# Kernel optimization log

Hardware: AMD Instinct MI355X
Metric: run time of the kernel (lower is better)

## Reference

```python
import jax, jax.numpy as jnp
import numpy as np

N_NODES = 100000
N_EDGES = 800000
N_GRAPHS = 4000
EMB = 128      # node_emb_dims
HID = 256      # hidden_dims
FP = 2048      # fingerprint_dims
FIELD_DIMS = {"atom_type": 120, "degree": 12, "charge": 10}


def setup_inputs() -> dict:
    key = jax.random.key(0)
    ks = iter(jax.random.split(key, 40))
    p = lambda shape: jax.random.normal(next(ks), shape, dtype=jnp.float32) * 0.02
    inp = {
        "atom_idx": jax.random.randint(next(ks), (N_NODES,), 0, FIELD_DIMS["atom_type"]),
        "degree_idx": jax.random.randint(next(ks), (N_NODES,), 0, FIELD_DIMS["degree"]),
        "charge_idx": jax.random.randint(next(ks), (N_NODES,), 0, FIELD_DIMS["charge"]),
        "edge_index": jax.random.randint(next(ks), (2, N_EDGES), 0, N_NODES),
        "batch": jnp.sort(jax.random.randint(next(ks), (N_NODES,), 0, N_GRAPHS)),
        "fingerprint": jax.random.normal(next(ks), (N_GRAPHS, FP), dtype=jnp.float32),
        # FFM projector params
        "emb_atom": p((FIELD_DIMS["atom_type"], EMB)),
        "emb_degree": p((FIELD_DIMS["degree"], EMB)),
        "emb_charge": p((FIELD_DIMS["charge"], EMB)),
        "proj_w1": p((3 * EMB, EMB)), "proj_b1": jnp.zeros((EMB,), jnp.float32),
        "proj_w2": p((EMB, EMB)), "proj_b2": jnp.zeros((EMB,), jnp.float32),
        # fingerprint linear
        "fp_w": p((FP, HID)), "fp_b": jnp.zeros((HID,), jnp.float32),
        # GCN layers
        "conv_w0": p((EMB, HID)), "conv_b0": jnp.zeros((HID,), jnp.float32),
        "conv_w1": p((HID, HID)), "conv_b1": jnp.zeros((HID,), jnp.float32),
        "conv_w2": p((HID, HID)), "conv_b2": jnp.zeros((HID,), jnp.float32),
        "conv_w3": p((HID, HID)), "conv_b3": jnp.zeros((HID,), jnp.float32),
        # head
        "lin1_w": p((2 * HID, HID // 2)), "lin1_b": jnp.zeros((HID // 2,), jnp.float32),
        "lin2_w": p((HID // 2, 1)), "lin2_b": jnp.zeros((1,), jnp.float32),
    }
    return inp


def gcn_conv(x, w, b, src, dst, n):
    # PyG GCNConv: linear, add self-loops, symmetric norm, scatter-add at dst, + bias
    xw = x @ w
    loop = jnp.arange(n)
    src_f = jnp.concatenate([src, loop])
    dst_f = jnp.concatenate([dst, loop])
    deg = jax.ops.segment_sum(jnp.ones_like(dst_f, dtype=x.dtype), dst_f, num_segments=n)
    dinv = jax.lax.rsqrt(deg)  # deg >= 1 thanks to self-loops
    norm = dinv[src_f] * dinv[dst_f]                       # [E+N]
    msg = xw[src_f] * norm[:, None]                        # [E+N, HID]
    return jax.ops.segment_sum(msg, dst_f, num_segments=n) + b


def reference(atom_idx, degree_idx, charge_idx, edge_index, batch, fingerprint,
              emb_atom, emb_degree, emb_charge,
              proj_w1, proj_b1, proj_w2, proj_b2, fp_w, fp_b,
              conv_w0, conv_b0, conv_w1, conv_b1, conv_w2, conv_b2, conv_w3, conv_b3,
              lin1_w, lin1_b, lin2_w, lin2_b):
    # FieldAwareFactorizationMachine projector (vectorized over all nodes)
    e = jnp.concatenate([emb_atom[atom_idx], emb_degree[degree_idx], emb_charge[charge_idx]], axis=-1)
    h = jax.nn.relu(e @ proj_w1 + proj_b1) @ proj_w2 + proj_b2   # [N, EMB]
    src, dst = edge_index[0], edge_index[1]
    for w, b in ((conv_w0, conv_b0), (conv_w1, conv_b1), (conv_w2, conv_b2), (conv_w3, conv_b3)):
        h = jax.nn.relu(gcn_conv(h, w, b, src, dst, N_NODES))
    pooled = jax.ops.segment_sum(h, batch, num_segments=N_GRAPHS)  # scatter sum pooling
    fp_emb = fingerprint @ fp_w + fp_b
    z = jnp.concatenate([fp_emb, pooled], axis=-1)                 # [B, 2*HID]
    z = jax.nn.relu(z @ lin1_w + lin1_b)
    return z @ lin2_w + lin2_b                                     # [B, 1]
```

## Files before the change

### kernel.cpp

```cpp
#include <hip/hip_runtime.h>
#include <stdint.h>

#define NN 100000
#define NE 800000
#define NG 4000
#define NBLK ((NN + 255) / 256)

typedef __attribute__((ext_vector_type(8))) short s16x8;
typedef __attribute__((ext_vector_type(4))) float f32x4;

__device__ __forceinline__ float b2f(unsigned short u) {
    return __uint_as_float(((unsigned int)u) << 16);
}
__device__ __forceinline__ unsigned short f2b(float f) {
    unsigned int x = __float_as_uint(f);
    x = x + 0x7FFFu + ((x >> 16) & 1u);
    return (unsigned short)(x >> 16);
}
__device__ __forceinline__ s16x8 cvt8(const float* __restrict__ p) {
    float4 a = *(const float4*)p;
    float4 b = *(const float4*)(p + 4);
    s16x8 r = {(short)f2b(a.x), (short)f2b(a.y), (short)f2b(a.z), (short)f2b(a.w),
               (short)f2b(b.x), (short)f2b(b.y), (short)f2b(b.z), (short)f2b(b.w)};
    return r;
}

__device__ __forceinline__ void gload16(const void* g, void* l) {
    __builtin_amdgcn_global_load_lds((const __attribute__((address_space(1))) unsigned int*)g,
                                     (__attribute__((address_space(3))) unsigned int*)l, 16, 0, 0);
}

__global__ void k_count(const int* __restrict__ dst, int* __restrict__ cnt) {
    int e = blockIdx.x * 256 + threadIdx.x;
    if (e < NE) atomicAdd(&cnt[dst[e]], 1);
}

__global__ void k_dinv(const int* __restrict__ cnt, float* __restrict__ dinv) {
    int n = blockIdx.x * 256 + threadIdx.x;
    if (n < NN) dinv[n] = rsqrtf((float)(cnt[n] + 1));
}

__global__ __launch_bounds__(256) void k_bsum(const int* __restrict__ cnt, int* __restrict__ bsum) {
    __shared__ int s[256];
    int i = blockIdx.x * 256 + threadIdx.x;
    s[threadIdx.x] = (i < NN) ? cnt[i] : 0;
    __syncthreads();
    for (int off = 128; off; off >>= 1) {
        if (threadIdx.x < off) s[threadIdx.x] += s[threadIdx.x + off];
        __syncthreads();
    }
    if (threadIdx.x == 0) bsum[blockIdx.x] = s[0];
}

__global__ __launch_bounds__(512) void k_bscan(const int* __restrict__ bsum, int* __restrict__ bpre) {
    __shared__ int s[512];
    int t = threadIdx.x;
    int v = (t < NBLK) ? bsum[t] : 0;
    s[t] = v;
    __syncthreads();
    for (int off = 1; off < 512; off <<= 1) {
        int u = (t >= off) ? s[t - off] : 0;
        __syncthreads();
        s[t] += u;
        __syncthreads();
    }
    if (t < NBLK) bpre[t] = s[t] - v;
}

__global__ __launch_bounds__(256) void k_rowptr(const int* __restrict__ cnt, const int* __restrict__ bpre,
                                                int* __restrict__ row_ptr, int* __restrict__ cursor) {
    __shared__ int s[256];
    int t = threadIdx.x;
    int i = blockIdx.x * 256 + t;
    int v = (i < NN) ? cnt[i] : 0;
    s[t] = v;
    __syncthreads();
    for (int off = 1; off < 256; off <<= 1) {
        int u = (t >= off) ? s[t - off] : 0;
        __syncthreads();
        s[t] += u;
        __syncthreads();
    }
    if (i < NN) {
        int excl = bpre[blockIdx.x] + s[t] - v;
        row_ptr[i] = excl;
        cursor[i] = excl;
        if (i == NN - 1) row_ptr[NN] = NE;
    }
}

__global__ void k_fill(const int* __restrict__ src, const int* __restrict__ dst,
                       int* __restrict__ cursor, int* __restrict__ colA) {
    int e = blockIdx.x * 256 + threadIdx.x;
    if (e < NE) {
        int d = dst[e];
        int p = atomicAdd(&cursor[d], 1);
        colA[p] = src[e];
    }
}

__global__ void k_t(const float* __restrict__ src, unsigned short* __restrict__ dst, int KN, int ln) {
    int i = blockIdx.x * 256 + threadIdx.x;
    if (i < KN) {
        int k = i >> ln, n = i & ((1 << ln) - 1);
        dst[(size_t)n * (KN >> ln) + k] = f2b(src[i]);
    }
}

__global__ void k_cvt(const float* __restrict__ src, unsigned short* __restrict__ dst, int n8) {
    int i = blockIdx.x * 256 + threadIdx.x;
    if (i < n8) *(s16x8*)&dst[(size_t)i * 8] = cvt8(&src[(size_t)i * 8]);
}

__global__ void k_binit(float* __restrict__ fe, const float* __restrict__ b) {
    int i = blockIdx.x * 256 + threadIdx.x;
    fe[i] = b[i & 255];
}

__global__ void k_z(const float* __restrict__ fe, unsigned short* __restrict__ zcat) {
    int i = blockIdx.x * 256 + threadIdx.x;
    int g = i >> 8, c = i & 255;
    zcat[(size_t)g * 512 + c] = f2b(fe[i]);
}

template <bool GATHER, bool BIAS, bool RELU, bool CBF16>
__global__ __launch_bounds__(256) void k_mm(
    const unsigned short* __restrict__ A, const unsigned short* __restrict__ Bt,
    void* __restrict__ Cv, const float* __restrict__ bias, int M, int N, int K,
    const int* __restrict__ ai, const int* __restrict__ di, const int* __restrict__ ci,
    const float* __restrict__ ea, const float* __restrict__ ed, const float* __restrict__ ec) {
    __shared__ unsigned short As[128 * 40];
    __shared__ unsigned short Bs[128 * 40];
    const int tid = threadIdx.x;
    const int row0 = blockIdx.x * 128, col0 = blockIdx.y * 128;
    const int lane = tid & 63, wid = tid >> 6;
    const int wrow = (wid >> 1) * 64, wcol = (wid & 1) * 64;
    const int lr = lane & 15, lk8 = (lane >> 4) * 8;

    const int sr = tid >> 1;
    const int skc = (tid & 1) * 16;
    const int agrow = row0 + sr;
    const int bgrow = col0 + sr;
    int ia = 0, idg = 0, ic = 0;
    if (GATHER && agrow < M) { ia = ai[agrow] * 128; idg = di[agrow] * 128; ic = ci[agrow] * 128; }

    f32x4 acc[4][4] = {};

    for (int kb = 0; kb < K; kb += 32) {
        if (kb) __syncthreads();
#pragma unroll
        for (int c = 0; c < 2; ++c) {
            int kloc = skc + c * 8;
            s16x8 v = {};
            if (agrow < M) {
                if (GATHER) {
                    int kg = kb + kloc;
                    const float* p = (kg < 128) ? (ea + ia + kg)
                                   : (kg < 256) ? (ed + idg + kg - 128)
                                                : (ec + ic + kg - 256);
                    v = cvt8(p);
                } else {
                    v = *(const s16x8*)&A[(size_t)agrow * K + kb + kloc];
                }
            }
            *(s16x8*)&As[sr * 40 + kloc] = v;
            s16x8 w = *(const s16x8*)&Bt[(size_t)bgrow * K + kb + kloc];
            *(s16x8*)&Bs[sr * 40 + kloc] = w;
        }
        __syncthreads();
        s16x8 af[4], bfr[4];
#pragma unroll
        for (int f = 0; f < 4; ++f)
            af[f] = *(const s16x8*)&As[(wrow + f * 16 + lr) * 40 + lk8];
#pragma unroll
        for (int f = 0; f < 4; ++f)
            bfr[f] = *(const s16x8*)&Bs[(wcol + f * 16 + lr) * 40 + lk8];
#pragma unroll
        for (int fm = 0; fm < 4; ++fm)
#pragma unroll
            for (int fn = 0; fn < 4; ++fn)
                acc[fm][fn] = __builtin_amdgcn_mfma_f32_16x16x32_bf16(af[fm], bfr[fn], acc[fm][fn], 0, 0, 0);
    }
#pragma unroll
    for (int fm = 0; fm < 4; ++fm) {
#pragma unroll
        for (int r = 0; r < 4; ++r) {
            int row = row0 + wrow + fm * 16 + (lane >> 4) * 4 + r;
            if (row < M) {
#pragma unroll
                for (int fn = 0; fn < 4; ++fn) {
                    int col = col0 + wcol + fn * 16 + lr;
                    float v = acc[fm][fn][r];
                    if (BIAS) v += bias[col];
                    if (RELU) v = fmaxf(v, 0.f);
                    if (CBF16) ((unsigned short*)Cv)[(size_t)row * N + col] = f2b(v);
                    else       ((float*)Cv)[(size_t)row * N + col] = v;
                }
            }
        }
    }
}

template <bool BIAS, bool RELU, bool CBF16, bool SPLITK>
__global__ __launch_bounds__(256) void k_mmA(
    const unsigned short* __restrict__ A, const unsigned short* __restrict__ Bt,
    void* __restrict__ Cv, const float* __restrict__ bias, int M, int N, int K, int kc) {
    __shared__ unsigned short As[128 * 32];
    __shared__ unsigned short Bs[128 * 32];
    const int tid = threadIdx.x;
    const int row0 = blockIdx.x * 128, col0 = blockIdx.y * 128;
    const int lane = tid & 63, wid = tid >> 6;
    const int wrow = (wid >> 1) * 64, wcol = (wid & 1) * 64;
    const int lr = lane & 15, lk8 = (lane >> 4) * 8;

    const int k0 = SPLITK ? blockIdx.z * kc : 0;
    const int k1 = SPLITK ? k0 + kc : K;

    const int sra = wid * 32 + (lane >> 2);
    const int sca = (lane & 3) * 8;
    const unsigned short* a0 = A + (size_t)min(row0 + sra, M - 1) * K + sca;
    const unsigned short* a1 = A + (size_t)min(row0 + sra + 16, M - 1) * K + sca;
    const unsigned short* b0 = Bt + (size_t)(col0 + sra) * K + sca;
    const unsigned short* b1 = Bt + (size_t)(col0 + sra + 16) * K + sca;
    unsigned short* lA0 = &As[(wid * 2 + 0) * 512];
    unsigned short* lA1 = &As[(wid * 2 + 1) * 512];
    unsigned short* lB0 = &Bs[(wid * 2 + 0) * 512];
    unsigned short* lB1 = &Bs[(wid * 2 + 1) * 512];

    f32x4 acc[4][4] = {};

    for (int kb = k0; kb < k1; kb += 32) {
        if (kb != k0) __syncthreads();
        gload16(a0 + kb, lA0);
        gload16(a1 + kb, lA1);
        gload16(b0 + kb, lB0);
        gload16(b1 + kb, lB1);
        __syncthreads();
        s16x8 af[4], bfr[4];
#pragma unroll
        for (int f = 0; f < 4; ++f)
            af[f] = *(const s16x8*)&As[(wrow + f * 16 + lr) * 32 + lk8];
#pragma unroll
        for (int f = 0; f < 4; ++f)
            bfr[f] = *(const s16x8*)&Bs[(wcol + f * 16 + lr) * 32 + lk8];
#pragma unroll
        for (int fm = 0; fm < 4; ++fm)
#pragma unroll
            for (int fn = 0; fn < 4; ++fn)
                acc[fm][fn] = __builtin_amdgcn_mfma_f32_16x16x32_bf16(af[fm], bfr[fn], acc[fm][fn], 0, 0, 0);
    }
#pragma unroll
    for (int fm = 0; fm < 4; ++fm) {
#pragma unroll
        for (int r = 0; r < 4; ++r) {
            int row = row0 + wrow + fm * 16 + (lane >> 4) * 4 + r;
            if (row < M) {
#pragma unroll
                for (int fn = 0; fn < 4; ++fn) {
                    int col = col0 + wcol + fn * 16 + lr;
                    float v = acc[fm][fn][r];
                    if (SPLITK) {
                        atomicAdd(&((float*)Cv)[(size_t)row * N + col], v);
                    } else {
                        if (BIAS) v += bias[col];
                        if (RELU) v = fmaxf(v, 0.f);
                        if (CBF16) ((unsigned short*)Cv)[(size_t)row * N + col] = f2b(v);
                        else       ((float*)Cv)[(size_t)row * N + col] = v;
                    }
                }
            }
        }
    }
}

template <int W, bool FUSE>
__global__ __launch_bounds__(256) void k_scat(const unsigned short* __restrict__ xw,
                                              unsigned short* __restrict__ hout,
                                              const float* __restrict__ dinv,
                                              const int* __restrict__ row_ptr,
                                              const int* __restrict__ colA,
                                              const float* __restrict__ bias) {
    constexpr int RPW = 1024 / W;
    constexpr int G = 64 / RPW;
    const int wid = threadIdx.x >> 6, lane = threadIdx.x & 63;
    const int v = blockIdx.x * 4 + wid;
    const int grp = lane / G, li = lane % G;
    const int c0 = li * 8;
    const float dv = dinv[v];
    float acc[8] = {};
    const int beg = row_ptr[v], end = row_ptr[v + 1];
    int p = beg + grp;
    for (; p + RPW < end; p += 2 * RPW) {
        int s0 = colA[p], s1 = colA[p + RPW];
        float w0 = dinv[s0] * dv, w1 = dinv[s1] * dv;
        s16x8 r0 = *(const s16x8*)&xw[(size_t)s0 * W + c0];
        s16x8 r1 = *(const s16x8*)&xw[(size_t)s1 * W + c0];
#pragma unroll
        for (int j = 0; j < 8; ++j) acc[j] = fmaf(b2f((unsigned short)r0[j]), w0, acc[j]);
#pragma unroll
        for (int j = 0; j < 8; ++j) acc[j] = fmaf(b2f((unsigned short)r1[j]), w1, acc[j]);
    }
    if (p < end) {
        int s0 = colA[p];
        float w0 = dinv[s0] * dv;
        s16x8 r0 = *(const s16x8*)&xw[(size_t)s0 * W + c0];
#pragma unroll
        for (int j = 0; j < 8; ++j) acc[j] = fmaf(b2f((unsigned short)r0[j]), w0, acc[j]);
    }
#pragma unroll
    for (int j = 0; j < 8; ++j) {
        if (RPW == 4) acc[j] += __shfl_xor(acc[j], 16);
        acc[j] += __shfl_xor(acc[j], 32);
    }
    s16x8 rs = *(const s16x8*)&xw[(size_t)v * W + c0];
    const float ws = dv * dv;
    unsigned short o[8];
#pragma unroll
    for (int j = 0; j < 8; ++j) {
        float x = fmaf(b2f((unsigned short)rs[j]), ws, acc[j]);
        if (FUSE) x = fmaxf(x + bias[c0 + j], 0.f);
        o[j] = f2b(x);
    }
    if (grp == 0) *(s16x8*)&hout[(size_t)v * W + c0] = *(const s16x8*)o;
}

__global__ __launch_bounds__(256) void k_scat256(const unsigned short* __restrict__ xw,
                                                 unsigned short* __restrict__ hout,
                                                 const float* __restrict__ dinv,
                                                 const int* __restrict__ row_ptr,
                                                 const int* __restrict__ colA,
                                                 const float* __restrict__ bias) {
    const int wid = threadIdx.x >> 6, lane = threadIdx.x & 63;
    const int v = blockIdx.x * 2 + (wid >> 1);
    const int cs = (wid & 1) * 128;
    const int grp = lane >> 4, li = lane & 15;
    const int c0 = cs + li * 8;
    const float dv = dinv[v];
    float acc[8] = {};
    const int beg = row_ptr[v], end = row_ptr[v + 1];
    int p = beg + grp;
    for (; p + 4 < end; p += 8) {
        int s0 = colA[p], s1 = colA[p + 4];
        float w0 = dinv[s0] * dv, w1 = dinv[s1] * dv;
        s16x8 r0 = *(const s16x8*)&xw[(size_t)s0 * 256 + c0];
        s16x8 r1 = *(const s16x8*)&xw[(size_t)s1 * 256 + c0];
#pragma unroll
        for (int j = 0; j < 8; ++j) acc[j] = fmaf(b2f((unsigned short)r0[j]), w0, acc[j]);
#pragma unroll
        for (int j = 0; j < 8; ++j) acc[j] = fmaf(b2f((unsigned short)r1[j]), w1, acc[j]);
    }
    if (p < end) {
        int s0 = colA[p];
        float w0 = dinv[s0] * dv;
        s16x8 r0 = *(const s16x8*)&xw[(size_t)s0 * 256 + c0];
#pragma unroll
        for (int j = 0; j < 8; ++j) acc[j] = fmaf(b2f((unsigned short)r0[j]), w0, acc[j]);
    }
#pragma unroll
    for (int j = 0; j < 8; ++j) {
        acc[j] += __shfl_xor(acc[j], 16);
        acc[j] += __shfl_xor(acc[j], 32);
    }
    s16x8 rs = *(const s16x8*)&xw[(size_t)v * 256 + c0];
    const float ws = dv * dv;
    unsigned short o[8];
#pragma unroll
    for (int j = 0; j < 8; ++j) {
        float x = fmaf(b2f((unsigned short)rs[j]), ws, acc[j]);
        x = fmaxf(x + bias[c0 + j], 0.f);
        o[j] = f2b(x);
    }
    if (grp == 0) *(s16x8*)&hout[(size_t)v * 256 + c0] = *(const s16x8*)o;
}

__global__ void k_bounds(const int* __restrict__ batch, int* __restrict__ gstart) {
    int n = blockIdx.x * 256 + threadIdx.x;
    if (n >= NN) return;
    int b = batch[n];
    if (n == 0) {
        for (int g = 0; g <= b; ++g) gstart[g] = 0;
    } else {
        int pb = batch[n - 1];
        if (pb != b)
            for (int g = pb + 1; g <= b; ++g) gstart[g] = n;
    }
    if (n == NN - 1) {
        for (int g = b + 1; g <= NG; ++g) gstart[g] = NN;
    }
}

__global__ __launch_bounds__(64) void k_pool(const unsigned short* __restrict__ h,
                                             const int* __restrict__ gstart,
                                             unsigned short* __restrict__ zcat) {
    int g = blockIdx.x;
    int lane = threadIdx.x;
    int c0 = lane * 4;
    int beg = gstart[g], end = gstart[g + 1];
    float a0 = 0.f, a1 = 0.f, a2 = 0.f, a3 = 0.f;
    for (int n = beg; n < end; ++n) {
        ushort4 r = *(const ushort4*)&h[(size_t)n * 256 + c0];
        a0 += b2f(r.x); a1 += b2f(r.y); a2 += b2f(r.z); a3 += b2f(r.w);
    }
    ushort4 o;
    o.x = f2b(a0); o.y = f2b(a1); o.z = f2b(a2); o.w = f2b(a3);
    *(ushort4*)&zcat[(size_t)g * 512 + 256 + c0] = o;
}

__global__ __launch_bounds__(256) void k_dot(const float* __restrict__ z1,
                                             const float* __restrict__ w2,
                                             const float* __restrict__ b2,
                                             float* __restrict__ out) {
    int wid = threadIdx.x >> 6, lane = threadIdx.x & 63;
    int g = blockIdx.x * 4 + wid;
    float s = z1[(size_t)g * 128 + lane] * w2[lane]
            + z1[(size_t)g * 128 + 64 + lane] * w2[64 + lane];
#pragma unroll
    for (int off = 32; off; off >>= 1) s += __shfl_xor(s, off);
    if (lane == 0) out[g] = s + b2[0];
}

extern "C" void kernel_launch(void* const* d_in, const int* in_sizes, int n_in,
                              void* d_out, int out_size, void* d_ws, size_t ws_size,
                              hipStream_t stream) {
    const int* atom_idx   = (const int*)d_in[0];
    const int* degree_idx = (const int*)d_in[1];
    const int* charge_idx = (const int*)d_in[2];
    const int* edge_index = (const int*)d_in[3];
    const int* batch      = (const int*)d_in[4];
    const float* fingerprint = (const float*)d_in[5];
    const float* emb_atom   = (const float*)d_in[6];
    const float* emb_degree = (const float*)d_in[7];
    const float* emb_charge = (const float*)d_in[8];
    const float* proj_w1 = (const float*)d_in[9];
    const float* proj_b1 = (const float*)d_in[10];
    const float* proj_w2 = (const float*)d_in[11];
    const float* proj_b2 = (const float*)d_in[12];
    const float* fp_w = (const float*)d_in[13];
    const float* fp_b = (const float*)d_in[14];
    const float* conv_w[4] = {(const float*)d_in[15], (const float*)d_in[17],
                              (const float*)d_in[19], (const float*)d_in[21]};
    const float* conv_b[4] = {(const float*)d_in[16], (const float*)d_in[18],
                              (const float*)d_in[20], (const float*)d_in[22]};
    const float* lin1_w = (const float*)d_in[23];
    const float* lin1_b = (const float*)d_in[24];
    const float* lin2_w = (const float*)d_in[25];
    const float* lin2_b = (const float*)d_in[26];
    float* out = (float*)d_out;

    const int* src = edge_index;
    const int* dst = edge_index + NE;

    char* p = (char*)d_ws;
    auto carve = [&](size_t bytes) { void* r = (void*)p; p += (bytes + 255) & ~(size_t)255; return r; };
    unsigned short* bufA = (unsigned short*)carve((size_t)NN * 256 * 2);
    unsigned short* bufB = (unsigned short*)carve((size_t)NN * 256 * 2);
    int*   cnt     = (int*)carve((size_t)NN * 4);
    float* dinv    = (float*)carve((size_t)NN * 4);
    int*   row_ptr = (int*)carve((size_t)(NN + 1) * 4);
    int*   cursor  = (int*)carve((size_t)(NN + 1) * 4);
    int*   colA    = (int*)carve((size_t)NE * 4);
    int*   gstart  = (int*)carve((size_t)(NG + 1) * 4);
    float* fp_emb  = (float*)carve((size_t)NG * 256 * 4);
    int*   bsum    = (int*)carve((size_t)NBLK * 4);
    int*   bpre    = (int*)carve((size_t)NBLK * 4);
    unsigned short* w1t  = (unsigned short*)carve((size_t)128 * 384 * 2);
    unsigned short* w2t  = (unsigned short*)carve((size_t)128 * 128 * 2);
    unsigned short* cwt[4];
    cwt[0] = (unsigned short*)carve((size_t)256 * 128 * 2);
    for (int l = 1; l < 4; ++l) cwt[l] = (unsigned short*)carve((size_t)256 * 256 * 2);
    unsigned short* fpwt = (unsigned short*)carve((size_t)256 * 2048 * 2);
    unsigned short* fpbf = (unsigned short*)carve((size_t)NG * 2048 * 2);
    unsigned short* l1wt = (unsigned short*)carve((size_t)128 * 512 * 2);
    unsigned short* zcat = (unsigned short*)carve((size_t)NG * 512 * 2);
    float* z1      = (float*)carve((size_t)NG * 128 * 4);

    hipMemsetAsync(cnt, 0, (size_t)NN * 4, stream);
    k_count<<<(NE + 255) / 256, 256, 0, stream>>>(dst, cnt);
    k_dinv<<<(NN + 255) / 256, 256, 0, stream>>>(cnt, dinv);
    k_bsum<<<NBLK, 256, 0, stream>>>(cnt, bsum);
    k_bscan<<<1, 512, 0, stream>>>(bsum, bpre);
    k_rowptr<<<NBLK, 256, 0, stream>>>(cnt, bpre, row_ptr, cursor);
    k_fill<<<(NE + 255) / 256, 256, 0, stream>>>(src, dst, cursor, colA);

    k_t<<<(49152 + 255) / 256, 256, 0, stream>>>(proj_w1, w1t, 49152, 7);
    k_t<<<(16384 + 255) / 256, 256, 0, stream>>>(proj_w2, w2t, 16384, 7);
    k_t<<<(32768 + 255) / 256, 256, 0, stream>>>(conv_w[0], cwt[0], 32768, 8);
    for (int l = 1; l < 4; ++l)
        k_t<<<(65536 + 255) / 256, 256, 0, stream>>>(conv_w[l], cwt[l], 65536, 8);
    k_t<<<(524288 + 255) / 256, 256, 0, stream>>>(fp_w, fpwt, 524288, 8);
    k_t<<<(65536 + 255) / 256, 256, 0, stream>>>(lin1_w, l1wt, 65536, 7);
    k_cvt<<<(NG * 2048 / 8 + 255) / 256, 256, 0, stream>>>(fingerprint, fpbf, NG * 2048 / 8);

    k_binit<<<NG, 256, 0, stream>>>(fp_emb, fp_b);
    k_mmA<false, false, false, true><<<dim3((NG + 127) / 128, 2, 4), 256, 0, stream>>>(
        fpbf, fpwt, fp_emb, nullptr, NG, 256, 2048, 512);
    k_z<<<NG, 256, 0, stream>>>(fp_emb, zcat);

    const int mg = (NN + 127) / 128;

    k_mm<true, true, true, true><<<dim3(mg, 1), 256, 0, stream>>>(
        nullptr, w1t, bufA, proj_b1, NN, 128, 384,
        atom_idx, degree_idx, charge_idx, emb_atom, emb_degree, emb_charge);
    k_mmA<true, false, true, false><<<dim3(mg, 1), 256, 0, stream>>>(
        bufA, w2t, bufB, proj_b2, NN, 128, 128, 0);

    k_scat<128, false><<<NN / 4, 256, 0, stream>>>(bufB, bufA, dinv, row_ptr, colA, nullptr);
    k_mmA<true, true, true, false><<<dim3(mg, 2), 256, 0, stream>>>(
        bufA, cwt[0], bufB, conv_b[0], NN, 256, 128, 0);

    for (int l = 1; l < 4; ++l) {
        k_mmA<false, false, true, false><<<dim3(mg, 2), 256, 0, stream>>>(
            bufB, cwt[l], bufA, nullptr, NN, 256, 256, 0);
        k_scat256<<<NN / 2, 256, 0, stream>>>(bufA, bufB, dinv, row_ptr, colA, conv_b[l]);
    }

    k_bounds<<<(NN + 255) / 256, 256, 0, stream>>>(batch, gstart);
    k_pool<<<NG, 64, 0, stream>>>(bufB, gstart, zcat);

    k_mmA<true, true, false, false><<<dim3((NG + 127) / 128, 1), 256, 0, stream>>>(
        zcat, l1wt, z1, lin1_b, NG, 128, 512, 0);
    k_dot<<<NG / 4, 256, 0, stream>>>(z1, lin2_w, lin2_b, out);
}
```

Before: 805.7 us.

## Fold source-side GCN normalization into GEMM epilogue, use packed adds in scatter

The per-edge weight dinv[src]*dinv[dst] is factored so the GEMMs producing xw multiply each row by dinv[row] in their epilogue. The scatter kernel then only sums bf16 rows with packed v_pk_add_f32 and scales once by dinv[dst] at the end, which removes the per-edge dinv gather and the per-element FMAs. The two scatter kernels are merged into a single template. Scaling before the bf16 rounding slightly changes numerics.

```diff
diff --git a/kernel.cpp b/kernel.cpp
--- a/kernel.cpp
+++ b/kernel.cpp
@@ -8,6 +8,7 @@
 
 typedef __attribute__((ext_vector_type(8))) short s16x8;
 typedef __attribute__((ext_vector_type(4))) float f32x4;
+typedef __attribute__((ext_vector_type(2))) float f32x2;
 
 __device__ __forceinline__ float b2f(unsigned short u) {
     return __uint_as_float(((unsigned int)u) << 16);
@@ -28,6 +29,18 @@
 __device__ __forceinline__ void gload16(const void* g, void* l) {
     __builtin_amdgcn_global_load_lds((const __attribute__((address_space(1))) unsigned int*)g,
                                      (__attribute__((address_space(3))) unsigned int*)l, 16, 0, 0);
+}
+
+__device__ __forceinline__ void acc8(f32x2* acc, s16x8 r) {
+    const unsigned int* u = (const unsigned int*)&r;
+#pragma unroll
+    for (int q = 0; q < 4; ++q) {
+        unsigned int w = u[q];
+        f32x2 x;
+        x[0] = __uint_as_float(w << 16);
+        x[1] = __uint_as_float(w & 0xFFFF0000u);
+        asm("v_pk_add_f32 %0, %1, %0" : "+v"(acc[q]) : "v"(x));
+    }
 }
 
 __global__ void k_count(const int* __restrict__ dst, int* __restrict__ cnt) {
@@ -201,10 +214,11 @@
     }
 }
 
-template <bool BIAS, bool RELU, bool CBF16, bool SPLITK>
+template <bool BIAS, bool RELU, bool CBF16, bool SPLITK, bool PRES>
 __global__ __launch_bounds__(256) void k_mmA(
     const unsigned short* __restrict__ A, const unsigned short* __restrict__ Bt,
-    void* __restrict__ Cv, const float* __restrict__ bias, int M, int N, int K, int kc) {
+    void* __restrict__ Cv, const float* __restrict__ bias, const float* __restrict__ pres,
+    int M, int N, int K, int kc) {
     __shared__ unsigned short As[128 * 32];
     __shared__ unsigned short Bs[128 * 32];
     const int tid = threadIdx.x;
@@ -255,6 +269,7 @@
         for (int r = 0; r < 4; ++r) {
             int row = row0 + wrow + fm * 16 + (lane >> 4) * 4 + r;
             if (row < M) {
+                float pr = PRES ? pres[row] : 1.f;
 #pragma unroll
                 for (int fn = 0; fn < 4; ++fn) {
                     int col = col0 + wcol + fn * 16 + lr;
@@ -264,6 +279,7 @@
                     } else {
                         if (BIAS) v += bias[col];
                         if (RELU) v = fmaxf(v, 0.f);
+                        if (PRES) v *= pr;
                         if (CBF16) ((unsigned short*)Cv)[(size_t)row * N + col] = f2b(v);
                         else       ((float*)Cv)[(size_t)row * N + col] = v;
                     }
@@ -273,104 +289,54 @@
     }
 }
 
-template <int W, bool FUSE>
-__global__ __launch_bounds__(256) void k_scat(const unsigned short* __restrict__ xw,
-                                              unsigned short* __restrict__ hout,
-                                              const float* __restrict__ dinv,
-                                              const int* __restrict__ row_ptr,
-                                              const int* __restrict__ colA,
-                                              const float* __restrict__ bias) {
-    constexpr int RPW = 1024 / W;
-    constexpr int G = 64 / RPW;
+template <int WPN, bool FUSE>
+__global__ __launch_bounds__(256) void k_scat2(const unsigned short* __restrict__ xw,
+                                               unsigned short* __restrict__ hout,
+                                               const float* __restrict__ dinv,
+                                               const int* __restrict__ row_ptr,
+                                               const int* __restrict__ colA,
+                                               const float* __restrict__ bias) {
+    constexpr int W = WPN * 128;
     const int wid = threadIdx.x >> 6, lane = threadIdx.x & 63;
-    const int v = blockIdx.x * 4 + wid;
-    const int grp = lane / G, li = lane % G;
-    const int c0 = li * 8;
-    const float dv = dinv[v];
-    float acc[8] = {};
-    const int beg = row_ptr[v], end = row_ptr[v + 1];
-    int p = beg + grp;
-    for (; p + RPW < end; p += 2 * RPW) {
-        int s0 = colA[p], s1 = colA[p + RPW];
-        float w0 = dinv[s0] * dv, w1 = dinv[s1] * dv;
-        s16x8 r0 = *(const s16x8*)&xw[(size_t)s0 * W + c0];
-        s16x8 r1 = *(const s16x8*)&xw[(size_t)s1 * W + c0];
-#pragma unroll
-        for (int j = 0; j < 8; ++j) acc[j] = fmaf(b2f((unsigned short)r0[j]), w0, acc[j]);
-#pragma unroll
-        for (int j = 0; j < 8; ++j) acc[j] = fmaf(b2f((unsigned short)r1[j]), w1, acc[j]);
-    }
-    if (p < end) {
-        int s0 = colA[p];
-        float w0 = dinv[s0] * dv;
-        s16x8 r0 = *(const s16x8*)&xw[(size_t)s0 * W + c0];
-#pragma unroll
-        for (int j = 0; j < 8; ++j) acc[j] = fmaf(b2f((unsigned short)r0[j]), w0, acc[j]);
-    }
-#pragma unroll
-    for (int j = 0; j < 8; ++j) {
-        if (RPW == 4) acc[j] += __shfl_xor(acc[j], 16);
-        acc[j] += __shfl_xor(acc[j], 32);
-    }
-    s16x8 rs = *(const s16x8*)&xw[(size_t)v * W + c0];
-    const float ws = dv * dv;
-    unsigned short o[8];
-#pragma unroll
-    for (int j = 0; j < 8; ++j) {
-        float x = fmaf(b2f((unsigned short)rs[j]), ws, acc[j]);
-        if (FUSE) x = fmaxf(x + bias[c0 + j], 0.f);
-        o[j] = f2b(x);
-    }
-    if (grp == 0) *(s16x8*)&hout[(size_t)v * W + c0] = *(const s16x8*)o;
-}
-
-__global__ __launch_bounds__(256) void k_scat256(const unsigned short* __restrict__ xw,
-                                                 unsigned short* __restrict__ hout,
-                                                 const float* __restrict__ dinv,
-                                                 const int* __restrict__ row_ptr,
-                                                 const int* __restrict__ colA,
-                                                 const float* __restrict__ bias) {
-    const int wid = threadIdx.x >> 6, lane = threadIdx.x & 63;
-    const int v = blockIdx.x * 2 + (wid >> 1);
-    const int cs = (wid & 1) * 128;
+    const int gw = blockIdx.x * 4 + wid;
+    const int v = (WPN == 2) ? (gw >> 1) : gw;
+    const int cs = (WPN == 2) ? (gw & 1) * 128 : 0;
     const int grp = lane >> 4, li = lane & 15;
     const int c0 = cs + li * 8;
-    const float dv = dinv[v];
-    float acc[8] = {};
+
+    f32x2 acc[4] = {};
     const int beg = row_ptr[v], end = row_ptr[v + 1];
     int p = beg + grp;
     for (; p + 4 < end; p += 8) {
         int s0 = colA[p], s1 = colA[p + 4];
-        float w0 = dinv[s0] * dv, w1 = dinv[s1] * dv;
-        s16x8 r0 = *(const s16x8*)&xw[(size_t)s0 * 256 + c0];
-        s16x8 r1 = *(const s16x8*)&xw[(size_t)s1 * 256 + c0];
-#pragma unroll
-        for (int j = 0; j < 8; ++j) acc[j] = fmaf(b2f((unsigned short)r0[j]), w0, acc[j]);
-#pragma unroll
-        for (int j = 0; j < 8; ++j) acc[j] = fmaf(b2f((unsigned short)r1[j]), w1, acc[j]);
+        s16x8 r0 = *(const s16x8*)&xw[(size_t)s0 * W + c0];
+        s16x8 r1 = *(const s16x8*)&xw[(size_t)s1 * W + c0];
+        acc8(acc, r0);
+        acc8(acc, r1);
     }
     if (p < end) {
         int s0 = colA[p];
-        float w0 = dinv[s0] * dv;
-        s16x8 r0 = *(const s16x8*)&xw[(size_t)s0 * 256 + c0];
-#pragma unroll
-        for (int j = 0; j < 8; ++j) acc[j] = fmaf(b2f((unsigned short)r0[j]), w0, acc[j]);
-    }
-#pragma unroll
-    for (int j = 0; j < 8; ++j) {
-        acc[j] += __shfl_xor(acc[j], 16);
-        acc[j] += __shfl_xor(acc[j], 32);
-    }
-    s16x8 rs = *(const s16x8*)&xw[(size_t)v * 256 + c0];
-    const float ws = dv * dv;
+        s16x8 r0 = *(const s16x8*)&xw[(size_t)s0 * W + c0];
+        acc8(acc, r0);
+    }
+
+    const float dv = dinv[v];
+    s16x8 rs = *(const s16x8*)&xw[(size_t)v * W + c0];
     unsigned short o[8];
 #pragma unroll
-    for (int j = 0; j < 8; ++j) {
-        float x = fmaf(b2f((unsigned short)rs[j]), ws, acc[j]);
-        x = fmaxf(x + bias[c0 + j], 0.f);
-        o[j] = f2b(x);
-    }
-    if (grp == 0) *(s16x8*)&hout[(size_t)v * 256 + c0] = *(const s16x8*)o;
+    for (int q = 0; q < 4; ++q) {
+#pragma unroll
+        for (int h = 0; h < 2; ++h) {
+            float a = acc[q][h];
+            a += __shfl_xor(a, 16);
+            a += __shfl_xor(a, 32);
+            a += b2f((unsigned short)rs[2 * q + h]);
+            a *= dv;
+            if (FUSE) a = fmaxf(a + bias[c0 + 2 * q + h], 0.f);
+            o[2 * q + h] = f2b(a);
+        }
+    }
+    if (grp == 0) *(s16x8*)&hout[(size_t)v * W + c0] = *(const s16x8*)o;
 }
 
 __global__ void k_bounds(const int* __restrict__ batch, int* __restrict__ gstart) {
@@ -492,8 +458,8 @@
     k_cvt<<<(NG * 2048 / 8 + 255) / 256, 256, 0, stream>>>(fingerprint, fpbf, NG * 2048 / 8);
 
     k_binit<<<NG, 256, 0, stream>>>(fp_emb, fp_b);
-    k_mmA<false, false, false, true><<<dim3((NG + 127) / 128, 2, 4), 256, 0, stream>>>(
-        fpbf, fpwt, fp_emb, nullptr, NG, 256, 2048, 512);
+    k_mmA<false, false, false, true, false><<<dim3((NG + 127) / 128, 2, 4), 256, 0, stream>>>(
+        fpbf, fpwt, fp_emb, nullptr, nullptr, NG, 256, 2048, 512);
     k_z<<<NG, 256, 0, stream>>>(fp_emb, zcat);
 
     const int mg = (NN + 127) / 128;
@@ -501,23 +467,23 @@
     k_mm<true, true, true, true><<<dim3(mg, 1), 256, 0, stream>>>(
         nullptr, w1t, bufA, proj_b1, NN, 128, 384,
         atom_idx, degree_idx, charge_idx, emb_atom, emb_degree, emb_charge);
-    k_mmA<true, false, true, false><<<dim3(mg, 1), 256, 0, stream>>>(
-        bufA, w2t, bufB, proj_b2, NN, 128, 128, 0);
-
-    k_scat<128, false><<<NN / 4, 256, 0, stream>>>(bufB, bufA, dinv, row_ptr, colA, nullptr);
-    k_mmA<true, true, true, false><<<dim3(mg, 2), 256, 0, stream>>>(
-        bufA, cwt[0], bufB, conv_b[0], NN, 256, 128, 0);
+    k_mmA<true, false, true, false, true><<<dim3(mg, 1), 256, 0, stream>>>(
+        bufA, w2t, bufB, proj_b2, dinv, NN, 128, 128, 0);
+
+    k_scat2<1, false><<<NN / 4, 256, 0, stream>>>(bufB, bufA, dinv, row_ptr, colA, nullptr);
+    k_mmA<true, true, true, false, false><<<dim3(mg, 2), 256, 0, stream>>>(
+        bufA, cwt[0], bufB, conv_b[0], nullptr, NN, 256, 128, 0);
 
     for (int l = 1; l < 4; ++l) {
-        k_mmA<false, false, true, false><<<dim3(mg, 2), 256, 0, stream>>>(
-            bufB, cwt[l], bufA, nullptr, NN, 256, 256, 0);
-        k_scat256<<<NN / 2, 256, 0, stream>>>(bufA, bufB, dinv, row_ptr, colA, conv_b[l]);
+        k_mmA<false, false, true, false, true><<<dim3(mg, 2), 256, 0, stream>>>(
+            bufB, cwt[l], bufA, nullptr, dinv, NN, 256, 256, 0);
+        k_scat2<2, true><<<NN / 2, 256, 0, stream>>>(bufA, bufB, dinv, row_ptr, colA, conv_b[l]);
     }
 
     k_bounds<<<(NN + 255) / 256, 256, 0, stream>>>(batch, gstart);
     k_pool<<<NG, 64, 0, stream>>>(bufB, gstart, zcat);
 
-    k_mmA<true, true, false, false><<<dim3((NG + 127) / 128, 1), 256, 0, stream>>>(
-        zcat, l1wt, z1, lin1_b, NG, 128, 512, 0);
+    k_mmA<true, true, false, false, false><<<dim3((NG + 127) / 128, 1), 256, 0, stream>>>(
+        zcat, l1wt, z1, lin1_b, nullptr, NG, 128, 512, 0);
     k_dot<<<NG / 4, 256, 0, stream>>>(z1, lin2_w, lin2_b, out);
 }
```

Result: faster. 789.8 us (-2.0%).
